# Optimization experiments

Measured on AMD Instinct MI355X. Metric: run time of the kernel, lower is better.

Reference implementation:

```python
import jax, jax.numpy as jnp
import numpy as np

N_HEAD, F_IN, F_OUT = 4, 768, 64
BS, N = 4, 2048


def setup_inputs() -> dict:
    key = jax.random.key(0)
    k_h, k_w, k_src, k_dst = jax.random.split(key, 4)
    # xavier_uniform bounds
    lim_w = float(np.sqrt(6.0 / (F_IN + F_OUT)))
    lim_a = float(np.sqrt(6.0 / (F_OUT + 1)))
    return {
        "h": jax.random.normal(k_h, (BS, N, F_IN), dtype=jnp.float32),
        "w": jax.random.uniform(k_w, (N_HEAD, F_IN, F_OUT), jnp.float32, -lim_w, lim_w),
        "a_src": jax.random.uniform(k_src, (N_HEAD, F_OUT, 1), jnp.float32, -lim_a, lim_a),
        "a_dst": jax.random.uniform(k_dst, (N_HEAD, F_OUT, 1), jnp.float32, -lim_a, lim_a),
        "bias": jnp.zeros((F_OUT,), dtype=jnp.float32),
    }


def reference(h, w, a_src, a_dst, bias):
    # h: [b, n, f_in]; w: [h, f_in, f_out]
    h_prime = jnp.einsum("bnf,hfo->bhno", h, w)          # [b, h, n, f_out]
    t = jnp.tanh(h_prime)
    attn_src = jnp.einsum("bhno,ho->bhn", t, a_src[..., 0])  # [b, h, n]
    attn_dst = jnp.einsum("bhno,ho->bhn", t, a_dst[..., 0])  # [b, h, n]
    # broadcast add: attn[b,h,i,j] = src[b,h,i] + dst[b,h,j]
    attn = attn_src[..., :, None] + attn_dst[..., None, :]   # [b, h, n, n]
    attn = jnp.where(attn >= 0, attn, 0.2 * attn)            # leaky_relu(0.2)
    attn = jax.nn.softmax(attn, axis=-1)
    out = jnp.einsum("bhij,bhjo->bhio", attn, h_prime)       # [b, h, n, f_out]
    return out + bias
```

## Files before the change

### kernel.cpp

```cpp
#include <hip/hip_runtime.h>
#include <hip/hip_bf16.h>

#define NHEAD 4
#define FIN   768
#define FOUT  64
#define BSZ   4
#define NSEQ  2048
#define BH    (BSZ*NHEAD)
#define LOG2E 1.44269504088896f

typedef __attribute__((ext_vector_type(8)))  short bf16x8;
typedef __attribute__((ext_vector_type(16))) float f32x16;
typedef __attribute__((ext_vector_type(8)))  unsigned short u16x8;
typedef __attribute__((ext_vector_type(4)))  unsigned short u16x4;
typedef __attribute__((ext_vector_type(4)))  unsigned u32x4;

__device__ __forceinline__ unsigned short f2bf(float f){
  unsigned b = __float_as_uint(f);
  return (unsigned short)((b + 0x7fffu + ((b >> 16) & 1u)) >> 16);
}
__device__ __forceinline__ float fexp2(float x){
#if __has_builtin(__builtin_amdgcn_exp2f)
  return __builtin_amdgcn_exp2f(x);
#else
  return exp2f(x);
#endif
}
__device__ __forceinline__ unsigned pkbf(float lo, float hi){
#if __has_builtin(__builtin_amdgcn_cvt_pk_bf16_f32)
  typedef __attribute__((ext_vector_type(2))) __bf16 bf2;
  union { bf2 v; unsigned u; } cv;
  cv.v = __builtin_amdgcn_cvt_pk_bf16_f32(lo, hi);
  return cv.u;
#else
  return (unsigned)f2bf(lo) | ((unsigned)f2bf(hi) << 16);
#endif
}
__device__ __forceinline__ float fast_tanh(float v){
  const float e = fexp2(v * (2.0f*LOG2E));
#if __has_builtin(__builtin_amdgcn_rcpf)
  return 1.0f - 2.0f*__builtin_amdgcn_rcpf(e + 1.0f);
#else
  return 1.0f - 2.0f/(e + 1.0f);
#endif
}
__device__ __forceinline__ void gll16(const void* g, void* l){
  __builtin_amdgcn_global_load_lds(
      (const __attribute__((address_space(1))) unsigned*)g,
      (__attribute__((address_space(3))) unsigned*)l, 16, 0, 0);
}

__global__ __launch_bounds__(512) void k_prep(
    const float* __restrict__ h, const float* __restrict__ w,
    unsigned short* __restrict__ h_bf, unsigned short* __restrict__ w_bf)
{
  const int tid = threadIdx.x;
  const int bid = blockIdx.x;
  if (bid < 1536){
    const int gid = bid*512 + tid;
    const int row = gid / 96;
    const int rem = gid - row*96;
    const int it  = rem >> 4, p = rem & 15;
    const float* src = h + (size_t)row*FIN + it*128 + ((p>>3)<<6)
                         + (((p & 7) ^ (row & 7)) << 3);
    const float4 a = *(const float4*)src;
    const float4 b = *(const float4*)(src + 4);
    u32x4 pk;
    pk[0] = pkbf(a.x, a.y); pk[1] = pkbf(a.z, a.w);
    pk[2] = pkbf(b.x, b.y); pk[3] = pkbf(b.z, b.w);
    *(u32x4*)((char*)h_bf + (size_t)gid*16) = pk;
  } else {
    const int wid = (bid - 1536)*512 + tid;
    const int p   = wid & 15, o = (wid >> 4) & 63, hi6 = wid >> 10;
    const int head = hi6 / 6, it = hi6 - head*6;
    const int k0 = it*128 + ((p>>3)<<6) + (((p & 7) ^ (o & 7)) << 3);
    const float* sw = w + (size_t)head*FIN*FOUT + (size_t)k0*FOUT + o;
    float r0 = sw[0*FOUT], r1 = sw[1*FOUT], r2 = sw[2*FOUT], r3 = sw[3*FOUT];
    float r4 = sw[4*FOUT], r5 = sw[5*FOUT], r6 = sw[6*FOUT], r7 = sw[7*FOUT];
    u32x4 pk;
    pk[0] = pkbf(r0, r1); pk[1] = pkbf(r2, r3);
    pk[2] = pkbf(r4, r5); pk[3] = pkbf(r6, r7);
    *(u32x4*)((char*)w_bf + (size_t)wid*16) = pk;
  }
}

__global__ __launch_bounds__(512, 4) void k_hprime(
    const unsigned short* __restrict__ h_bf, const unsigned short* __restrict__ w_bf,
    const float* __restrict__ a_src, const float* __restrict__ a_dst,
    unsigned short* __restrict__ hpz2, float* __restrict__ srcv,
    float* __restrict__ dstv)
{
  __shared__ __align__(16) char smem[65536];
  float* psumS = (float*)(smem + 16384);
  float* psumD = (float*)(smem + 16896);
  char*  Tt    = smem + 32768;

  const int tid  = threadIdx.x;
  const int bid  = blockIdx.x;
  const int bh1  = (bid & 7) | (((bid >> 3) & 1) << 3);
  const int head = bh1 & 3;
  const int jbase = (bid >> 4) << 6;
  const int i0a   = (bh1 >> 2)*NSEQ + jbase;
  const int wave = tid >> 6, lane = tid & 63;
  const int wm = wave & 1, wn = (wave >> 1) & 1, kw = wave >> 2;
  const int l32 = lane & 31, h32 = lane >> 5;

  f32x16 acc = {0,0,0,0,0,0,0,0,0,0,0,0,0,0,0,0};

  const int rowL = wave*4 + (lane >> 4);
  const int p16  = lane & 15;
  const char* sA = (const char*)h_bf + ((size_t)(i0a + rowL)*96 + p16)*16;
  const char* sB = (const char*)w_bf + (size_t)(head*6)*16384 + rowL*256 + p16*16;

  {
    char* AbW = smem +         wave*1024;
    char* BbW = smem + 32768 + wave*1024;
    gll16(sA,         AbW);
    gll16(sA + 49152, AbW + 8192);
    gll16(sB,         BbW);
    gll16(sB + 8192,  BbW + 8192);
  }
  __syncthreads();

  for (int it = 0; it < 6; ++it){
    const int bb = it & 1;
    char* Ab = smem +         bb*16384;
    char* Bb = smem + 32768 + bb*16384;
    if (it < 5){
      char* AbW = smem +         (bb^1)*16384 + wave*1024;
      char* BbW = smem + 32768 + (bb^1)*16384 + wave*1024;
      const char* sAi = sA + (size_t)(it+1)*256;
      const char* sBi = sB + (size_t)(it+1)*16384;
      gll16(sAi,         AbW);
      gll16(sAi + 49152, AbW + 8192);
      gll16(sBi,         BbW);
      gll16(sBi + 8192,  BbW + 8192);
    }
    #pragma unroll
    for (int s = 0; s < 4; ++s){
      const int slot = (((s*2 + h32) ^ (l32 & 7)) << 4);
      bf16x8 av = *(const bf16x8*)(Ab + (wm*32 + l32)*256 + kw*128 + slot);
      bf16x8 bv = *(const bf16x8*)(Bb + (wn*32 + l32)*256 + kw*128 + slot);
      acc = __builtin_amdgcn_mfma_f32_32x32x16_bf16(av, bv, acc, 0, 0, 0);
    }
    __syncthreads();
  }

  if (kw == 1) *(f32x16*)(smem + (size_t)((wave & 3)*64 + lane)*64) = acc;
  __syncthreads();
  if (kw == 0){
    acc += *(const f32x16*)(smem + (size_t)((wave & 3)*64 + lane)*64);
    const float as = a_src[head*64 + wn*32 + l32];
    const float ad = a_dst[head*64 + wn*32 + l32];
    #pragma unroll
    for (int rb2 = 0; rb2 < 4; ++rb2){
      const int jb = wm*32 + rb2*8 + h32*4;
      u16x4 c4;
      #pragma unroll
      for (int q = 0; q < 4; ++q){
        const float v = acc[rb2*4 + q];
        c4[q] = f2bf(v);
        const float t = fast_tanh(v);
        float ps = t*as, pd = t*ad;
        ps += __shfl_xor(ps, 1);  ps += __shfl_xor(ps, 2);  ps += __shfl_xor(ps, 4);
        ps += __shfl_xor(ps, 8);  ps += __shfl_xor(ps, 16);
        pd += __shfl_xor(pd, 1);  pd += __shfl_xor(pd, 2);  pd += __shfl_xor(pd, 4);
        pd += __shfl_xor(pd, 8);  pd += __shfl_xor(pd, 16);
        if (l32 == 0){
          psumS[(jb + q)*2 + wn] = ps;
          psumD[(jb + q)*2 + wn] = pd;
        }
      }
      const int orow = wn*32 + l32;
      const int slot = ((jb >> 3) & 7) ^ (orow & 7);
      *(u16x4*)(Tt + orow*128 + slot*16 + (jb & 7)*2) = c4;
    }
  }
  __syncthreads();

  {
    const int o = tid & 63, c = tid >> 6;
    u16x8 val = *(const u16x8*)(Tt + o*128 + ((c ^ (o & 7)) << 4));
    *(u16x8*)((char*)hpz2 + ((size_t)(bh1*256 + (jbase >> 3) + c)*64 + o)*16) = val;
  }
  if (tid < 64){
    srcv[(size_t)bh1*NSEQ + jbase + tid] = (psumS[tid*2] + psumS[tid*2 + 1]) * LOG2E;
    dstv[(size_t)bh1*NSEQ + jbase + tid] = (psumD[tid*2] + psumD[tid*2 + 1]) * LOG2E;
  }
}

__global__ __launch_bounds__(512, 4) void k_attn(
    const unsigned short* __restrict__ hpz2, const float* __restrict__ srcv,
    const float* __restrict__ dstv, const float* __restrict__ bias,
    float* __restrict__ out)
{
  __shared__ __align__(16) char smem[33792];
  float* Lbuf = (float*)(smem + 32768);

  const int tid = threadIdx.x;
  const int bid = blockIdx.x;
  const int bh  = (bid & 7) | (((bid >> 3) & 1) << 3);
  const int i0  = (bid >> 4) << 6;
  const int wave = tid >> 6, lane = tid & 63;
  const int wm = wave & 1, jw = wave >> 1;
  const int l32 = lane & 31, h32 = lane >> 5;

  const float s2 = srcv[(size_t)bh*NSEQ + i0 + wm*32 + l32];
  const float u_ = s2;
  const float v_ = 0.2f*s2;
  const float* dptr = dstv + (size_t)bh*NSEQ;

  const u16x8* gp = (const u16x8*)((const char*)hpz2 + (size_t)bh*256*64*16);

  f32x16 accO0 = {0,0,0,0,0,0,0,0,0,0,0,0,0,0,0,0};
  f32x16 accO1 = {0,0,0,0,0,0,0,0,0,0,0,0,0,0,0,0};
  float lpart = 0.f;

  *(u16x8*)(smem + tid*16)         = gp[tid];
  *(u16x8*)(smem + (tid + 512)*16) = gp[tid + 512];
  __syncthreads();

  for (int w = 0; w < 16; ++w){
    char* cur = smem + (w & 1)*16384;
    char* nxt = smem + ((w + 1) & 1)*16384;
    u16x8 r0, r1;
    if (w < 15){
      r0 = gp[(w+1)*1024 + tid];
      r1 = gp[(w+1)*1024 + tid + 512];
    }
    #pragma unroll
    for (int stl = 0; stl < 2; ++stl){
      const int Jl = jw*4 + stl*2 + h32;
      const int j0 = (w*16 + Jl)*8;
      float4 d0 = *(const float4*)(dptr + j0);
      float4 d1 = *(const float4*)(dptr + j0 + 4);
      float e0,e1,e2,e3,e4,e5,e6,e7;
      e0 = fexp2(fmaxf(u_ + d0.x, fmaf(0.2f, d0.x, v_)));
      e1 = fexp2(fmaxf(u_ + d0.y, fmaf(0.2f, d0.y, v_)));
      e2 = fexp2(fmaxf(u_ + d0.z, fmaf(0.2f, d0.z, v_)));
      e3 = fexp2(fmaxf(u_ + d0.w, fmaf(0.2f, d0.w, v_)));
      e4 = fexp2(fmaxf(u_ + d1.x, fmaf(0.2f, d1.x, v_)));
      e5 = fexp2(fmaxf(u_ + d1.y, fmaf(0.2f, d1.y, v_)));
      e6 = fexp2(fmaxf(u_ + d1.z, fmaf(0.2f, d1.z, v_)));
      e7 = fexp2(fmaxf(u_ + d1.w, fmaf(0.2f, d1.w, v_)));
      lpart += ((e0+e1)+(e2+e3)) + ((e4+e5)+(e6+e7));
      u32x4 pk;
      pk[0] = pkbf(e0, e1); pk[1] = pkbf(e2, e3);
      pk[2] = pkbf(e4, e5); pk[3] = pkbf(e6, e7);
      const bf16x8 pA = __builtin_bit_cast(bf16x8, pk);
      const bf16x8 bv0 = *(const bf16x8*)(cur + (Jl*64 +      l32)*16);
      const bf16x8 bv1 = *(const bf16x8*)(cur + (Jl*64 + 32 + l32)*16);
      accO0 = __builtin_amdgcn_mfma_f32_32x32x16_bf16(pA, bv0, accO0, 0, 0, 0);
      accO1 = __builtin_amdgcn_mfma_f32_32x32x16_bf16(pA, bv1, accO1, 0, 0, 0);
    }
    if (w < 15){
      *(u16x8*)(nxt + tid*16)         = r0;
      *(u16x8*)(nxt + (tid + 512)*16) = r1;
    }
    __syncthreads();
  }

  lpart += __shfl_xor(lpart, 32);
  if (lane < 32) Lbuf[(wm*4 + jw)*32 + l32] = lpart;

  const float4 bia = *(const float4*)(bias + (tid & 15)*4);
  #pragma unroll
  for (int ph = 0; ph < 2; ++ph){
    __syncthreads();
    if (wm == ph){
      float* ob = (float*)smem;
      #pragma unroll
      for (int reg = 0; reg < 16; ++reg){
        const int m = (reg & 3) + 8*(reg >> 2) + 4*h32;
        ob[(jw*32 + m)*64 +      l32] = accO0[reg];
        ob[(jw*32 + m)*64 + 32 + l32] = accO1[reg];
      }
    }
    __syncthreads();
    {
      const int i = tid >> 4, o4 = (tid & 15)*4;
      const float* ob = (const float*)smem;
      float4 v0 = *(const float4*)(ob + (0*32 + i)*64 + o4);
      float4 v1 = *(const float4*)(ob + (1*32 + i)*64 + o4);
      float4 v2 = *(const float4*)(ob + (2*32 + i)*64 + o4);
      float4 v3 = *(const float4*)(ob + (3*32 + i)*64 + o4);
      const float l = Lbuf[(ph*4+0)*32 + i] + Lbuf[(ph*4+1)*32 + i]
                    + Lbuf[(ph*4+2)*32 + i] + Lbuf[(ph*4+3)*32 + i];
      const float r = 1.f / l;
      float4 res;
      res.x = (v0.x + v1.x + v2.x + v3.x)*r + bia.x;
      res.y = (v0.y + v1.y + v2.y + v3.y)*r + bia.y;
      res.z = (v0.z + v1.z + v2.z + v3.z)*r + bia.z;
      res.w = (v0.w + v1.w + v2.w + v3.w)*r + bia.w;
      *(float4*)(out + ((size_t)bh*NSEQ + i0 + ph*32 + i)*64 + o4) = res;
    }
  }
}

extern "C" void kernel_launch(void* const* d_in, const int* in_sizes, int n_in,
                              void* d_out, int out_size, void* d_ws, size_t ws_size,
                              hipStream_t stream)
{
  const float* h     = (const float*)d_in[0];
  const float* w     = (const float*)d_in[1];
  const float* a_src = (const float*)d_in[2];
  const float* a_dst = (const float*)d_in[3];
  const float* bias  = (const float*)d_in[4];
  float* out = (float*)d_out;

  char* ws = (char*)d_ws;
  unsigned short* hpz2 = (unsigned short*)ws;
  float* srcv = (float*)(ws + (4u<<20));
  float* dstv = (float*)(ws + (4u<<20) + (128u<<10));
  unsigned short* h_bf = (unsigned short*)(ws + (8u<<20));
  unsigned short* w_bf = (unsigned short*)(ws + (8u<<20) + 12582912u);

  k_prep<<<1584, 512, 0, stream>>>(h, w, h_bf, w_bf);
  k_hprime<<<512, 512, 0, stream>>>(h_bf, w_bf, a_src, a_dst, hpz2, srcv, dstv);
  k_attn<<<512, 512, 0, stream>>>(hpz2, srcv, dstv, bias, out);
}
```

Before: 121.8 us.

## Fuse prep, projection and attention kernels into one persistent kernel with grid barriers

Merges the three kernels (bf16 conversion, h' projection with attention scores, attention softmax-matmul) into a single 512-block kernel. The stages are separated by software grid-wide barriers built on atomic counters, and the counters are reset by a memset before launch. The aim is to remove kernel launch gaps and tail effects between stages. The risk is spin-wait overhead, and deadlock if all 512 blocks cannot be co-resident, since the code relies on 4 blocks per CU via launch bounds.

```diff
diff --git a/kernel.cpp b/kernel.cpp
--- a/kernel.cpp
+++ b/kernel.cpp
@@ -50,249 +50,258 @@
       (__attribute__((address_space(3))) unsigned*)l, 16, 0, 0);
 }
 
-__global__ __launch_bounds__(512) void k_prep(
+__device__ __forceinline__ void gbar(unsigned* c, unsigned target){
+  __syncthreads();
+  if (threadIdx.x == 0){
+    __threadfence();
+    __hip_atomic_fetch_add(c, 1u, __ATOMIC_RELAXED, __HIP_MEMORY_SCOPE_AGENT);
+    int guard = 0;
+    while (__hip_atomic_load(c, __ATOMIC_RELAXED, __HIP_MEMORY_SCOPE_AGENT) < target
+           && ++guard < (1 << 24))
+      __builtin_amdgcn_s_sleep(2);
+  }
+  __syncthreads();
+  __threadfence();
+}
+
+__global__ __launch_bounds__(512, 4) void k_fused(
     const float* __restrict__ h, const float* __restrict__ w,
-    unsigned short* __restrict__ h_bf, unsigned short* __restrict__ w_bf)
+    const float* __restrict__ a_src, const float* __restrict__ a_dst,
+    const float* __restrict__ bias, float* __restrict__ out,
+    unsigned short* __restrict__ hpz2, float* __restrict__ srcv,
+    float* __restrict__ dstv, unsigned short* __restrict__ h_bf,
+    unsigned short* __restrict__ w_bf, unsigned* __restrict__ bar)
 {
+  __shared__ __align__(16) char smem[65536];
   const int tid = threadIdx.x;
   const int bid = blockIdx.x;
-  if (bid < 1536){
-    const int gid = bid*512 + tid;
-    const int row = gid / 96;
-    const int rem = gid - row*96;
-    const int it  = rem >> 4, p = rem & 15;
-    const float* src = h + (size_t)row*FIN + it*128 + ((p>>3)<<6)
-                         + (((p & 7) ^ (row & 7)) << 3);
-    const float4 a = *(const float4*)src;
-    const float4 b = *(const float4*)(src + 4);
-    u32x4 pk;
-    pk[0] = pkbf(a.x, a.y); pk[1] = pkbf(a.z, a.w);
-    pk[2] = pkbf(b.x, b.y); pk[3] = pkbf(b.z, b.w);
-    *(u32x4*)((char*)h_bf + (size_t)gid*16) = pk;
-  } else {
-    const int wid = (bid - 1536)*512 + tid;
-    const int p   = wid & 15, o = (wid >> 4) & 63, hi6 = wid >> 10;
-    const int head = hi6 / 6, it = hi6 - head*6;
-    const int k0 = it*128 + ((p>>3)<<6) + (((p & 7) ^ (o & 7)) << 3);
-    const float* sw = w + (size_t)head*FIN*FOUT + (size_t)k0*FOUT + o;
-    float r0 = sw[0*FOUT], r1 = sw[1*FOUT], r2 = sw[2*FOUT], r3 = sw[3*FOUT];
-    float r4 = sw[4*FOUT], r5 = sw[5*FOUT], r6 = sw[6*FOUT], r7 = sw[7*FOUT];
-    u32x4 pk;
-    pk[0] = pkbf(r0, r1); pk[1] = pkbf(r2, r3);
-    pk[2] = pkbf(r4, r5); pk[3] = pkbf(r6, r7);
-    *(u32x4*)((char*)w_bf + (size_t)wid*16) = pk;
+  const int wave = tid >> 6, lane = tid & 63;
+  const int l32 = lane & 31, h32 = lane >> 5;
+
+  {
+    #pragma unroll
+    for (int c = 0; c < 3; ++c){
+      const int gid = c*262144 + bid*512 + tid;
+      const int row = gid / 96;
+      const int rem = gid - row*96;
+      const int it  = rem >> 4, p = rem & 15;
+      const float* src = h + (size_t)row*FIN + it*128 + ((p>>3)<<6)
+                           + (((p & 7) ^ (row & 7)) << 3);
+      const float4 a = *(const float4*)src;
+      const float4 b = *(const float4*)(src + 4);
+      u32x4 pk;
+      pk[0] = pkbf(a.x, a.y); pk[1] = pkbf(a.z, a.w);
+      pk[2] = pkbf(b.x, b.y); pk[3] = pkbf(b.z, b.w);
+      *(u32x4*)((char*)h_bf + (size_t)gid*16) = pk;
+    }
+    if (bid < 48){
+      const int wid = bid*512 + tid;
+      const int p   = wid & 15, o = (wid >> 4) & 63, hi6 = wid >> 10;
+      const int hd  = hi6 / 6, it = hi6 - hd*6;
+      const int k0 = it*128 + ((p>>3)<<6) + (((p & 7) ^ (o & 7)) << 3);
+      const float* sw = w + (size_t)hd*FIN*FOUT + (size_t)k0*FOUT + o;
+      float r0 = sw[0*FOUT], r1 = sw[1*FOUT], r2 = sw[2*FOUT], r3 = sw[3*FOUT];
+      float r4 = sw[4*FOUT], r5 = sw[5*FOUT], r6 = sw[6*FOUT], r7 = sw[7*FOUT];
+      u32x4 pk;
+      pk[0] = pkbf(r0, r1); pk[1] = pkbf(r2, r3);
+      pk[2] = pkbf(r4, r5); pk[3] = pkbf(r6, r7);
+      *(u32x4*)((char*)w_bf + (size_t)wid*16) = pk;
+    }
   }
-}
-
-__global__ __launch_bounds__(512, 4) void k_hprime(
-    const unsigned short* __restrict__ h_bf, const unsigned short* __restrict__ w_bf,
-    const float* __restrict__ a_src, const float* __restrict__ a_dst,
-    unsigned short* __restrict__ hpz2, float* __restrict__ srcv,
-    float* __restrict__ dstv)
-{
-  __shared__ __align__(16) char smem[65536];
-  float* psumS = (float*)(smem + 16384);
-  float* psumD = (float*)(smem + 16896);
-  char*  Tt    = smem + 32768;
-
-  const int tid  = threadIdx.x;
-  const int bid  = blockIdx.x;
-  const int bh1  = (bid & 7) | (((bid >> 3) & 1) << 3);
-  const int head = bh1 & 3;
-  const int jbase = (bid >> 4) << 6;
-  const int i0a   = (bh1 >> 2)*NSEQ + jbase;
-  const int wave = tid >> 6, lane = tid & 63;
-  const int wm = wave & 1, wn = (wave >> 1) & 1, kw = wave >> 2;
-  const int l32 = lane & 31, h32 = lane >> 5;
-
-  f32x16 acc = {0,0,0,0,0,0,0,0,0,0,0,0,0,0,0,0};
-
-  const int rowL = wave*4 + (lane >> 4);
-  const int p16  = lane & 15;
-  const char* sA = (const char*)h_bf + ((size_t)(i0a + rowL)*96 + p16)*16;
-  const char* sB = (const char*)w_bf + (size_t)(head*6)*16384 + rowL*256 + p16*16;
+  gbar(bar + 0, 512);
 
   {
-    char* AbW = smem +         wave*1024;
-    char* BbW = smem + 32768 + wave*1024;
-    gll16(sA,         AbW);
-    gll16(sA + 49152, AbW + 8192);
-    gll16(sB,         BbW);
-    gll16(sB + 8192,  BbW + 8192);
+    float* psumS = (float*)(smem + 16384);
+    float* psumD = (float*)(smem + 16896);
+    char*  Tt    = smem + 32768;
+
+    const int bh1  = (bid & 7) | (((bid >> 3) & 1) << 3);
+    const int head = bh1 & 3;
+    const int jbase = (bid >> 4) << 6;
+    const int i0a   = (bh1 >> 2)*NSEQ + jbase;
+    const int wm = wave & 1, wn = (wave >> 1) & 1, kw = wave >> 2;
+
+    f32x16 acc = {0,0,0,0,0,0,0,0,0,0,0,0,0,0,0,0};
+
+    const int rowL = wave*4 + (lane >> 4);
+    const int p16  = lane & 15;
+    const char* sA = (const char*)h_bf + ((size_t)(i0a + rowL)*96 + p16)*16;
+    const char* sB = (const char*)w_bf + (size_t)(head*6)*16384 + rowL*256 + p16*16;
+
+    {
+      char* AbW = smem +         wave*1024;
+      char* BbW = smem + 32768 + wave*1024;
+      gll16(sA,         AbW);
+      gll16(sA + 49152, AbW + 8192);
+      gll16(sB,         BbW);
+      gll16(sB + 8192,  BbW + 8192);
+    }
+    __syncthreads();
+
+    for (int it = 0; it < 6; ++it){
+      const int bb = it & 1;
+      char* Ab = smem +         bb*16384;
+      char* Bb = smem + 32768 + bb*16384;
+      if (it < 5){
+        char* AbW = smem +         (bb^1)*16384 + wave*1024;
+        char* BbW = smem + 32768 + (bb^1)*16384 + wave*1024;
+        const char* sAi = sA + (size_t)(it+1)*256;
+        const char* sBi = sB + (size_t)(it+1)*16384;
+        gll16(sAi,         AbW);
+        gll16(sAi + 49152, AbW + 8192);
+        gll16(sBi,         BbW);
+        gll16(sBi + 8192,  BbW + 8192);
+      }
+      #pragma unroll
+      for (int s = 0; s < 4; ++s){
+        const int slot = (((s*2 + h32) ^ (l32 & 7)) << 4);
+        bf16x8 av = *(const bf16x8*)(Ab + (wm*32 + l32)*256 + kw*128 + slot);
+        bf16x8 bv = *(const bf16x8*)(Bb + (wn*32 + l32)*256 + kw*128 + slot);
+        acc = __builtin_amdgcn_mfma_f32_32x32x16_bf16(av, bv, acc, 0, 0, 0);
+      }
+      __syncthreads();
+    }
+
+    if (kw == 1) *(f32x16*)(smem + (size_t)((wave & 3)*64 + lane)*64) = acc;
+    __syncthreads();
+    if (kw == 0){
+      acc += *(const f32x16*)(smem + (size_t)((wave & 3)*64 + lane)*64);
+      const float as = a_src[head*64 + wn*32 + l32];
+      const float ad = a_dst[head*64 + wn*32 + l32];
+      #pragma unroll
+      for (int rb2 = 0; rb2 < 4; ++rb2){
+        const int jb = wm*32 + rb2*8 + h32*4;
+        u16x4 c4;
+        #pragma unroll
+        for (int q = 0; q < 4; ++q){
+          const float v = acc[rb2*4 + q];
+          c4[q] = f2bf(v);
+          const float t = fast_tanh(v);
+          float ps = t*as, pd = t*ad;
+          ps += __shfl_xor(ps, 1);  ps += __shfl_xor(ps, 2);  ps += __shfl_xor(ps, 4);
+          ps += __shfl_xor(ps, 8);  ps += __shfl_xor(ps, 16);
+          pd += __shfl_xor(pd, 1);  pd += __shfl_xor(pd, 2);  pd += __shfl_xor(pd, 4);
+          pd += __shfl_xor(pd, 8);  pd += __shfl_xor(pd, 16);
+          if (l32 == 0){
+            psumS[(jb + q)*2 + wn] = ps;
+            psumD[(jb + q)*2 + wn] = pd;
+          }
+        }
+        const int orow = wn*32 + l32;
+        const int slot = ((jb >> 3) & 7) ^ (orow & 7);
+        *(u16x4*)(Tt + orow*128 + slot*16 + (jb & 7)*2) = c4;
+      }
+    }
+    __syncthreads();
+
+    {
+      const int o = tid & 63, c = tid >> 6;
+      u16x8 val = *(const u16x8*)(Tt + o*128 + ((c ^ (o & 7)) << 4));
+      *(u16x8*)((char*)hpz2 + ((size_t)(bh1*256 + (jbase >> 3) + c)*64 + o)*16) = val;
+    }
+    if (tid < 64){
+      srcv[(size_t)bh1*NSEQ + jbase + tid] = (psumS[tid*2] + psumS[tid*2 + 1]) * LOG2E;
+      dstv[(size_t)bh1*NSEQ + jbase + tid] = (psumD[tid*2] + psumD[tid*2 + 1]) * LOG2E;
+    }
   }
-  __syncthreads();
-
-  for (int it = 0; it < 6; ++it){
-    const int bb = it & 1;
-    char* Ab = smem +         bb*16384;
-    char* Bb = smem + 32768 + bb*16384;
-    if (it < 5){
-      char* AbW = smem +         (bb^1)*16384 + wave*1024;
-      char* BbW = smem + 32768 + (bb^1)*16384 + wave*1024;
-      const char* sAi = sA + (size_t)(it+1)*256;
-      const char* sBi = sB + (size_t)(it+1)*16384;
-      gll16(sAi,         AbW);
-      gll16(sAi + 49152, AbW + 8192);
-      gll16(sBi,         BbW);
-      gll16(sBi + 8192,  BbW + 8192);
-    }
+  gbar(bar + 1, 512);
+
+  {
+    float* Lbuf = (float*)(smem + 32768);
+
+    const int bh  = (bid & 7) | (((bid >> 3) & 1) << 3);
+    const int i0  = (bid >> 4) << 6;
+    const int wm = wave & 1, jw = wave >> 1;
+
+    const float s2 = srcv[(size_t)bh*NSEQ + i0 + wm*32 + l32];
+    const float u_ = s2;
+    const float v_ = 0.2f*s2;
+    const float* dptr = dstv + (size_t)bh*NSEQ;
+
+    const u16x8* gp = (const u16x8*)((const char*)hpz2 + (size_t)bh*256*64*16);
+
+    f32x16 accO0 = {0,0,0,0,0,0,0,0,0,0,0,0,0,0,0,0};
+    f32x16 accO1 = {0,0,0,0,0,0,0,0,0,0,0,0,0,0,0,0};
+    float lpart = 0.f;
+
+    *(u16x8*)(smem + tid*16)         = gp[tid];
+    *(u16x8*)(smem + (tid + 512)*16) = gp[tid + 512];
+    __syncthreads();
+
+    for (int wt = 0; wt < 16; ++wt){
+      char* cur = smem + (wt & 1)*16384;
+      char* nxt = smem + ((wt + 1) & 1)*16384;
+      u16x8 r0, r1;
+      if (wt < 15){
+        r0 = gp[(wt+1)*1024 + tid];
+        r1 = gp[(wt+1)*1024 + tid + 512];
+      }
+      #pragma unroll
+      for (int stl = 0; stl < 2; ++stl){
+        const int Jl = jw*4 + stl*2 + h32;
+        const int j0 = (wt*16 + Jl)*8;
+        float4 d0 = *(const float4*)(dptr + j0);
+        float4 d1 = *(const float4*)(dptr + j0 + 4);
+        float e0,e1,e2,e3,e4,e5,e6,e7;
+        e0 = fexp2(fmaxf(u_ + d0.x, fmaf(0.2f, d0.x, v_)));
+        e1 = fexp2(fmaxf(u_ + d0.y, fmaf(0.2f, d0.y, v_)));
+        e2 = fexp2(fmaxf(u_ + d0.z, fmaf(0.2f, d0.z, v_)));
+        e3 = fexp2(fmaxf(u_ + d0.w, fmaf(0.2f, d0.w, v_)));
+        e4 = fexp2(fmaxf(u_ + d1.x, fmaf(0.2f, d1.x, v_)));
+        e5 = fexp2(fmaxf(u_ + d1.y, fmaf(0.2f, d1.y, v_)));
+        e6 = fexp2(fmaxf(u_ + d1.z, fmaf(0.2f, d1.z, v_)));
+        e7 = fexp2(fmaxf(u_ + d1.w, fmaf(0.2f, d1.w, v_)));
+        lpart += ((e0+e1)+(e2+e3)) + ((e4+e5)+(e6+e7));
+        u32x4 pk;
+        pk[0] = pkbf(e0, e1); pk[1] = pkbf(e2, e3);
+        pk[2] = pkbf(e4, e5); pk[3] = pkbf(e6, e7);
+        const bf16x8 pA = __builtin_bit_cast(bf16x8, pk);
+        const bf16x8 bv0 = *(const bf16x8*)(cur + (Jl*64 +      l32)*16);
+        const bf16x8 bv1 = *(const bf16x8*)(cur + (Jl*64 + 32 + l32)*16);
+        accO0 = __builtin_amdgcn_mfma_f32_32x32x16_bf16(pA, bv0, accO0, 0, 0, 0);
+        accO1 = __builtin_amdgcn_mfma_f32_32x32x16_bf16(pA, bv1, accO1, 0, 0, 0);
+      }
+      if (wt < 15){
+        *(u16x8*)(nxt + tid*16)         = r0;
+        *(u16x8*)(nxt + (tid + 512)*16) = r1;
+      }
+      __syncthreads();
+    }
+
+    lpart += __shfl_xor(lpart, 32);
+    if (lane < 32) Lbuf[(wm*4 + jw)*32 + l32] = lpart;
+
+    const float4 bia = *(const float4*)(bias + (tid & 15)*4);
     #pragma unroll
-    for (int s = 0; s < 4; ++s){
-      const int slot = (((s*2 + h32) ^ (l32 & 7)) << 4);
-      bf16x8 av = *(const bf16x8*)(Ab + (wm*32 + l32)*256 + kw*128 + slot);
-      bf16x8 bv = *(const bf16x8*)(Bb + (wn*32 + l32)*256 + kw*128 + slot);
-      acc = __builtin_amdgcn_mfma_f32_32x32x16_bf16(av, bv, acc, 0, 0, 0);
-    }
-    __syncthreads();
-  }
-
-  if (kw == 1) *(f32x16*)(smem + (size_t)((wave & 3)*64 + lane)*64) = acc;
-  __syncthreads();
-  if (kw == 0){
-    acc += *(const f32x16*)(smem + (size_t)((wave & 3)*64 + lane)*64);
-    const float as = a_src[head*64 + wn*32 + l32];
-    const float ad = a_dst[head*64 + wn*32 + l32];
-    #pragma unroll
-    for (int rb2 = 0; rb2 < 4; ++rb2){
-      const int jb = wm*32 + rb2*8 + h32*4;
-      u16x4 c4;
-      #pragma unroll
-      for (int q = 0; q < 4; ++q){
-        const float v = acc[rb2*4 + q];
-        c4[q] = f2bf(v);
-        const float t = fast_tanh(v);
-        float ps = t*as, pd = t*ad;
-        ps += __shfl_xor(ps, 1);  ps += __shfl_xor(ps, 2);  ps += __shfl_xor(ps, 4);
-        ps += __shfl_xor(ps, 8);  ps += __shfl_xor(ps, 16);
-        pd += __shfl_xor(pd, 1);  pd += __shfl_xor(pd, 2);  pd += __shfl_xor(pd, 4);
-        pd += __shfl_xor(pd, 8);  pd += __shfl_xor(pd, 16);
-        if (l32 == 0){
-          psumS[(jb + q)*2 + wn] = ps;
-          psumD[(jb + q)*2 + wn] = pd;
+    for (int ph = 0; ph < 2; ++ph){
+      __syncthreads();
+      if (wm == ph){
+        float* ob = (float*)smem;
+        #pragma unroll
+        for (int reg = 0; reg < 16; ++reg){
+          const int m = (reg & 3) + 8*(reg >> 2) + 4*h32;
+          ob[(jw*32 + m)*64 +      l32] = accO0[reg];
+          ob[(jw*32 + m)*64 + 32 + l32] = accO1[reg];
         }
       }
-      const int orow = wn*32 + l32;
-      const int slot = ((jb >> 3) & 7) ^ (orow & 7);
-      *(u16x4*)(Tt + orow*128 + slot*16 + (jb & 7)*2) = c4;
-    }
-  }
-  __syncthreads();
-
-  {
-    const int o = tid & 63, c = tid >> 6;
-    u16x8 val = *(const u16x8*)(Tt + o*128 + ((c ^ (o & 7)) << 4));
-    *(u16x8*)((char*)hpz2 + ((size_t)(bh1*256 + (jbase >> 3) + c)*64 + o)*16) = val;
-  }
-  if (tid < 64){
-    srcv[(size_t)bh1*NSEQ + jbase + tid] = (psumS[tid*2] + psumS[tid*2 + 1]) * LOG2E;
-    dstv[(size_t)bh1*NSEQ + jbase + tid] = (psumD[tid*2] + psumD[tid*2 + 1]) * LOG2E;
-  }
-}
-
-__global__ __launch_bounds__(512, 4) void k_attn(
-    const unsigned short* __restrict__ hpz2, const float* __restrict__ srcv,
-    const float* __restrict__ dstv, const float* __restrict__ bias,
-    float* __restrict__ out)
-{
-  __shared__ __align__(16) char smem[33792];
-  float* Lbuf = (float*)(smem + 32768);
-
-  const int tid = threadIdx.x;
-  const int bid = blockIdx.x;
-  const int bh  = (bid & 7) | (((bid >> 3) & 1) << 3);
-  const int i0  = (bid >> 4) << 6;
-  const int wave = tid >> 6, lane = tid & 63;
-  const int wm = wave & 1, jw = wave >> 1;
-  const int l32 = lane & 31, h32 = lane >> 5;
-
-  const float s2 = srcv[(size_t)bh*NSEQ + i0 + wm*32 + l32];
-  const float u_ = s2;
-  const float v_ = 0.2f*s2;
-  const float* dptr = dstv + (size_t)bh*NSEQ;
-
-  const u16x8* gp = (const u16x8*)((const char*)hpz2 + (size_t)bh*256*64*16);
-
-  f32x16 accO0 = {0,0,0,0,0,0,0,0,0,0,0,0,0,0,0,0};
-  f32x16 accO1 = {0,0,0,0,0,0,0,0,0,0,0,0,0,0,0,0};
-  float lpart = 0.f;
-
-  *(u16x8*)(smem + tid*16)         = gp[tid];
-  *(u16x8*)(smem + (tid + 512)*16) = gp[tid + 512];
-  __syncthreads();
-
-  for (int w = 0; w < 16; ++w){
-    char* cur = smem + (w & 1)*16384;
-    char* nxt = smem + ((w + 1) & 1)*16384;
-    u16x8 r0, r1;
-    if (w < 15){
-      r0 = gp[(w+1)*1024 + tid];
-      r1 = gp[(w+1)*1024 + tid + 512];
-    }
-    #pragma unroll
-    for (int stl = 0; stl < 2; ++stl){
-      const int Jl = jw*4 + stl*2 + h32;
-      const int j0 = (w*16 + Jl)*8;
-      float4 d0 = *(const float4*)(dptr + j0);
-      float4 d1 = *(const float4*)(dptr + j0 + 4);
-      float e0,e1,e2,e3,e4,e5,e6,e7;
-      e0 = fexp2(fmaxf(u_ + d0.x, fmaf(0.2f, d0.x, v_)));
-      e1 = fexp2(fmaxf(u_ + d0.y, fmaf(0.2f, d0.y, v_)));
-      e2 = fexp2(fmaxf(u_ + d0.z, fmaf(0.2f, d0.z, v_)));
-      e3 = fexp2(fmaxf(u_ + d0.w, fmaf(0.2f, d0.w, v_)));
-      e4 = fexp2(fmaxf(u_ + d1.x, fmaf(0.2f, d1.x, v_)));
-      e5 = fexp2(fmaxf(u_ + d1.y, fmaf(0.2f, d1.y, v_)));
-      e6 = fexp2(fmaxf(u_ + d1.z, fmaf(0.2f, d1.z, v_)));
-      e7 = fexp2(fmaxf(u_ + d1.w, fmaf(0.2f, d1.w, v_)));
-      lpart += ((e0+e1)+(e2+e3)) + ((e4+e5)+(e6+e7));
-      u32x4 pk;
-      pk[0] = pkbf(e0, e1); pk[1] = pkbf(e2, e3);
-      pk[2] = pkbf(e4, e5); pk[3] = pkbf(e6, e7);
-      const bf16x8 pA = __builtin_bit_cast(bf16x8, pk);
-      const bf16x8 bv0 = *(const bf16x8*)(cur + (Jl*64 +      l32)*16);
-      const bf16x8 bv1 = *(const bf16x8*)(cur + (Jl*64 + 32 + l32)*16);
-      accO0 = __builtin_amdgcn_mfma_f32_32x32x16_bf16(pA, bv0, accO0, 0, 0, 0);
-      accO1 = __builtin_amdgcn_mfma_f32_32x32x16_bf16(pA, bv1, accO1, 0, 0, 0);
-    }
-    if (w < 15){
-      *(u16x8*)(nxt + tid*16)         = r0;
-      *(u16x8*)(nxt + (tid + 512)*16) = r1;
-    }
-    __syncthreads();
-  }
-
-  lpart += __shfl_xor(lpart, 32);
-  if (lane < 32) Lbuf[(wm*4 + jw)*32 + l32] = lpart;
-
-  const float4 bia = *(const float4*)(bias + (tid & 15)*4);
-  #pragma unroll
-  for (int ph = 0; ph < 2; ++ph){
-    __syncthreads();
-    if (wm == ph){
-      float* ob = (float*)smem;
-      #pragma unroll
-      for (int reg = 0; reg < 16; ++reg){
-        const int m = (reg & 3) + 8*(reg >> 2) + 4*h32;
-        ob[(jw*32 + m)*64 +      l32] = accO0[reg];
-        ob[(jw*32 + m)*64 + 32 + l32] = accO1[reg];
-      }
-    }
-    __syncthreads();
-    {
-      const int i = tid >> 4, o4 = (tid & 15)*4;
-      const float* ob = (const float*)smem;
-      float4 v0 = *(const float4*)(ob + (0*32 + i)*64 + o4);
-      float4 v1 = *(const float4*)(ob + (1*32 + i)*64 + o4);
-      float4 v2 = *(const float4*)(ob + (2*32 + i)*64 + o4);
-      float4 v3 = *(const float4*)(ob + (3*32 + i)*64 + o4);
-      const float l = Lbuf[(ph*4+0)*32 + i] + Lbuf[(ph*4+1)*32 + i]
-                    + Lbuf[(ph*4+2)*32 + i] + Lbuf[(ph*4+3)*32 + i];
-      const float r = 1.f / l;
-      float4 res;
-      res.x = (v0.x + v1.x + v2.x + v3.x)*r + bia.x;
-      res.y = (v0.y + v1.y + v2.y + v3.y)*r + bia.y;
-      res.z = (v0.z + v1.z + v2.z + v3.z)*r + bia.z;
-      res.w = (v0.w + v1.w + v2.w + v3.w)*r + bia.w;
-      *(float4*)(out + ((size_t)bh*NSEQ + i0 + ph*32 + i)*64 + o4) = res;
+      __syncthreads();
+      {
+        const int i = tid >> 4, o4 = (tid & 15)*4;
+        const float* ob = (const float*)smem;
+        float4 v0 = *(const float4*)(ob + (0*32 + i)*64 + o4);
+        float4 v1 = *(const float4*)(ob + (1*32 + i)*64 + o4);
+        float4 v2 = *(const float4*)(ob + (2*32 + i)*64 + o4);
+        float4 v3 = *(const float4*)(ob + (3*32 + i)*64 + o4);
+        const float l = Lbuf[(ph*4+0)*32 + i] + Lbuf[(ph*4+1)*32 + i]
+                      + Lbuf[(ph*4+2)*32 + i] + Lbuf[(ph*4+3)*32 + i];
+        const float r = 1.f / l;
+        float4 res;
+        res.x = (v0.x + v1.x + v2.x + v3.x)*r + bia.x;
+        res.y = (v0.y + v1.y + v2.y + v3.y)*r + bia.y;
+        res.z = (v0.z + v1.z + v2.z + v3.z)*r + bia.z;
+        res.w = (v0.w + v1.w + v2.w + v3.w)*r + bia.w;
+        *(float4*)(out + ((size_t)bh*NSEQ + i0 + ph*32 + i)*64 + o4) = res;
+      }
     }
   }
 }
@@ -314,8 +323,9 @@
   float* dstv = (float*)(ws + (4u<<20) + (128u<<10));
   unsigned short* h_bf = (unsigned short*)(ws + (8u<<20));
   unsigned short* w_bf = (unsigned short*)(ws + (8u<<20) + 12582912u);
-
-  k_prep<<<1584, 512, 0, stream>>>(h, w, h_bf, w_bf);
-  k_hprime<<<512, 512, 0, stream>>>(h_bf, w_bf, a_src, a_dst, hpz2, srcv, dstv);
-  k_attn<<<512, 512, 0, stream>>>(hpz2, srcv, dstv, bias, out);
-}
+  unsigned* bar = (unsigned*)(ws + (24u<<20));
+
+  hipMemsetAsync(bar, 0, 256, stream);
+  k_fused<<<512, 512, 0, stream>>>(h, w, a_src, a_dst, bias, out,
+                                   hpz2, srcv, dstv, h_bf, w_bf, bar);
+}
```

Result: slower. 319.3 us (+162.1%).
